# Kernel tuning notes

Hardware: AMD Instinct MI355X
Metric: run time of the kernel (lower is better)

## Reference

```python
import jax, jax.numpy as jnp
import numpy as np

B, C, M, NH, F_, W = 2, 8, 8, 8, 1024, 512  # batch, channels, attention_maps, heads, features, frames
HD = F_ // NH
EXP = 4


def _conv(x, w, b):
    y = jax.lax.conv_general_dilated(x, w, (1, 1), 'SAME',
                                     dimension_numbers=('NCHW', 'OIHW', 'NCHW'))
    return y + b[None, :, None, None]


def _rope(x):
    # x: (..., seq, d); lucidrains-style interleaved rotary embedding
    d, n = x.shape[-1], x.shape[-2]
    inv = 1.0 / (10000.0 ** (jnp.arange(0, d, 2, dtype=jnp.float32) / d))
    fr = jnp.repeat(jnp.arange(n, dtype=jnp.float32)[:, None] * inv[None, :], 2, axis=-1)
    cos, sin = jnp.cos(fr), jnp.sin(fr)
    xr = jnp.stack((-x[..., 1::2], x[..., 0::2]), axis=-1).reshape(x.shape)
    return x * cos + xr * sin


def _mcln(x, w, b, eps=1e-5):
    # MultichannelLayerNorm: normalize over features axis (axis=2 of B,C,F,W)
    mu = jnp.mean(x, axis=2, keepdims=True)
    var = jnp.var(x, axis=2, keepdims=True)
    return (x - mu) / jnp.sqrt(var + eps) * w[None, :, :, None] + b[None, :, :, None]


def _mclin(x, w_pw):
    # MultichannelLinear positionwise: per-channel matmul over features
    return jnp.einsum('bcfw,cgf->bcgw', x, w_pw)


def setup_inputs() -> dict:
    key = jax.random.key(0)
    ks = jax.random.split(key, 24)
    s = 0.02
    d = {
        'x': jax.random.normal(ks[0], (B, C, F_, W), jnp.float32),
        'prev_qk': jax.random.normal(ks[1], (B, M, NH, W, W), jnp.float32),
        'qconv_w': jax.random.normal(ks[2], (M, C, 3, 3), jnp.float32) * s,
        'qconv_b': jnp.zeros((M,), jnp.float32),
        'q_pw': jax.random.normal(ks[3], (M, F_, F_), jnp.float32) * s,
        'kconv_w': jax.random.normal(ks[4], (M, C, 3, 3), jnp.float32) * s,
        'kconv_b': jnp.zeros((M,), jnp.float32),
        'k_pw': jax.random.normal(ks[5], (M, F_, F_), jnp.float32) * s,
        'vconv_w': jax.random.normal(ks[6], (M, C, 3, 3), jnp.float32) * s,
        'vconv_b': jnp.zeros((M,), jnp.float32),
        'v_pw': jax.random.normal(ks[7], (M, F_, F_), jnp.float32) * s,
        'o_pw': jax.random.normal(ks[8], (M, F_, F_), jnp.float32) * s,
        'o_dw': jax.random.normal(ks[9], (M, M), jnp.float32) * s,
        'oproj_w': jax.random.normal(ks[10], (C, C + M, 3, 3), jnp.float32) * s,
        'oproj_b': jnp.zeros((C,), jnp.float32),
        'n1_w': jnp.ones((C, F_), jnp.float32),
        'n1_b': jnp.zeros((C, F_), jnp.float32),
        'c1_w': jax.random.normal(ks[11], (C * EXP, C, 3, 3), jnp.float32) * s,
        'c1_b': jnp.zeros((C * EXP,), jnp.float32),
        'c2_w': jax.random.normal(ks[12], (C, C * EXP, 3, 3), jnp.float32) * s,
        'c2_b': jnp.zeros((C,), jnp.float32),
        'n2_w': jnp.ones((C, F_), jnp.float32),
        'n2_b': jnp.zeros((C, F_), jnp.float32),
    }
    return d


def _encoder(x, prev_qk, qconv_w, qconv_b, q_pw, kconv_w, kconv_b, k_pw,
             vconv_w, vconv_b, v_pw, o_pw, o_dw, oproj_w, oproj_b,
             n1_w, n1_b, c1_w, c1_b, c2_w, c2_b, n2_w, n2_b):
    b, c, h, w = x.shape

    def heads(y):  # (B,M,F,W) -> (B,M,NH,W,HD)
        return y.transpose(0, 1, 3, 2).reshape(b, M, w, NH, HD).transpose(0, 1, 3, 2, 4)

    q = _rope(heads(_mclin(_conv(x, qconv_w, qconv_b), q_pw)))
    k = _rope(heads(_mclin(_conv(x, kconv_w, kconv_b), k_pw)))
    v = heads(_mclin(_conv(x, vconv_w, vconv_b), v_pw))

    qk = jnp.einsum('bmnqd,bmnkd->bmnqk', q, k) / jnp.sqrt(jnp.float32(h))
    qk = qk + prev_qk
    a = jnp.einsum('bmnqk,bmnkd->bmnqd', jax.nn.softmax(qk, axis=-1), v)
    a = a.transpose(0, 1, 3, 2, 4).reshape(b, M, w, NH * HD).transpose(0, 1, 3, 2)  # (B,M,F,W)
    a = jnp.einsum('bcfw,dc->bdfw', _mclin(a, o_pw), o_dw)  # depthwise o_linear
    z = _conv(jnp.concatenate((x, a), axis=1), oproj_w, oproj_b)

    hid = _mcln(x + z, n1_w, n1_b)  # dropout is identity in eval
    z2 = _conv(jax.nn.gelu(_conv(hid, c1_w, c1_b), approximate=False), c2_w, c2_b)
    out = _mcln(hid + z2, n2_w, n2_b)
    return out, qk


def reference(x, prev_qk, qconv_w, qconv_b, q_pw, kconv_w, kconv_b, k_pw,
              vconv_w, vconv_b, v_pw, o_pw, o_dw, oproj_w, oproj_b,
              n1_w, n1_b, c1_w, c1_b, c2_w, c2_b, n2_w, n2_b):
    out, qk = _encoder(x, prev_qk, qconv_w, qconv_b, q_pw, kconv_w, kconv_b, k_pw,
                       vconv_w, vconv_b, v_pw, o_pw, o_dw, oproj_w, oproj_b,
                       n1_w, n1_b, c1_w, c1_b, c2_w, c2_b, n2_w, n2_b)
    return (out, out, qk)
```

## Files before the change

### kernel.cpp

```cpp
#include <hip/hip_runtime.h>
#include <math.h>

#define B_ 2
#define C_ 8
#define M_ 8
#define NH_ 8
#define F_ 1024
#define W_ 512
#define HD_ 128
#define FW 524288L
#define PF_ 1026
#define PW_ 514

typedef __bf16 bf16_t;
typedef __bf16 bf16x8 __attribute__((ext_vector_type(8)));
typedef __bf16 bf16x4 __attribute__((ext_vector_type(4)));
typedef float f32x4 __attribute__((ext_vector_type(4)));

__device__ __forceinline__ void gload16(const void* g, void* l) {
    __builtin_amdgcn_global_load_lds(
        (const __attribute__((address_space(1))) unsigned int*)g,
        (__attribute__((address_space(3))) unsigned int*)l,
        16, 0, 0);
}

__device__ __forceinline__ float gelu_f(float v) {
    return 0.5f * v * (1.0f + erff(v * 0.70710678118f));
}

__device__ __forceinline__ void xcd_swz3(int& bx, int& by, int& bz) {
    const int nwg = gridDim.x * gridDim.y * gridDim.z;
    int orig = blockIdx.x + gridDim.x * (blockIdx.y + gridDim.y * blockIdx.z);
    orig = (orig & 7) * (nwg >> 3) + (orig >> 3);
    bx = orig % gridDim.x;
    int t = orig / gridDim.x;
    by = t % gridDim.y;
    bz = t / gridDim.y;
}

__global__ __launch_bounds__(256)
void prep_k(const float* __restrict__ q_pw, const float* __restrict__ k_pw,
            const float* __restrict__ v_pw, const float* __restrict__ o_pw,
            const float* __restrict__ x,
            const float* __restrict__ qw, const float* __restrict__ kw,
            const float* __restrict__ vw, const float* __restrict__ ow,
            const float* __restrict__ c1w, const float* __restrict__ c2w,
            const float* __restrict__ qb, const float* __restrict__ kb,
            const float* __restrict__ vb,
            bf16_t* __restrict__ W4, bf16_t* __restrict__ px,
            bf16_t* __restrict__ a_qkv, bf16_t* __restrict__ a_op,
            bf16_t* __restrict__ a_c1, bf16_t* __restrict__ a_c2,
            float* __restrict__ bias_qkv,
            bf16_t* __restrict__ p8a, bf16_t* __restrict__ p8b, bf16_t* __restrict__ p32)
{
    const int bid = blockIdx.x, tid = threadIdx.x;
    if (bid < 32768) {
        long i = (long)bid * 256 + tid;
        const int wsel = (int)(i >> 21);
        const long off = i & 2097151L;
        const float* src = (wsel == 0) ? q_pw : (wsel == 1) ? k_pw : (wsel == 2) ? v_pw : o_pw;
        float4 v = ((const float4*)src)[off];
        bf16x4 r = { (bf16_t)v.x, (bf16_t)v.y, (bf16_t)v.z, (bf16_t)v.w };
        *(bf16x4*)&W4[i * 4] = r;
    } else if (bid < 36889) {
        long i = (long)(bid - 32768) * 256 + tid;
        if (i >= (long)B_ * PF_ * PW_) return;
        int wc = (int)(i % PW_);
        long t = i / PW_;
        int fr = (int)(t % PF_);
        int b  = (int)(t / PF_);
        bf16x8 v = {};
        if (fr >= 1 && fr <= F_ && wc >= 1 && wc <= W_) {
            const float* s = x + (long)b * 8 * FW + (long)(fr - 1) * W_ + (wc - 1);
            #pragma unroll
            for (int c = 0; c < 8; ++c) v[c] = (bf16_t)s[c * FW];
        }
        *(bf16x8*)&px[i * 8] = v;
    } else if (bid < 36961) {
        int sub = bid - 36889;
        int mode = sub / 18;
        int i = (sub % 18) * 256 + tid;
        if (mode == 0) {
            if (i < 3072) {
                int k = i & 31, co = (i >> 5) & 31, df = i >> 10;
                int tap = k >> 3, ci = k & 7;
                float v = 0.f;
                if (tap < 3) {
                    if (co < 8)       v = qw[((co * 8 + ci) * 3 + df) * 3 + tap];
                    else if (co < 16) v = kw[(((co - 8) * 8 + ci) * 3 + df) * 3 + tap];
                    else if (co < 24) v = vw[(((co - 16) * 8 + ci) * 3 + df) * 3 + tap];
                }
                a_qkv[i] = (bf16_t)v;
            }
            if (i < 32) bias_qkv[i] = (i < 8) ? qb[i] : (i < 16) ? kb[i - 8] : (i < 24) ? vb[i - 16] : 0.f;
        } else if (mode == 1) {
            if (i < 3072) {
                int k = i & 63, co = (i >> 6) & 15, df = i >> 10;
                int src = k >> 5, r = k & 31, tap = r >> 3, ci = src * 8 + (r & 7);
                float v = 0.f;
                if (co < 8 && tap < 3) v = ow[((co * 16 + ci) * 3 + df) * 3 + tap];
                a_op[i] = (bf16_t)v;
            }
        } else if (mode == 2) {
            if (i < 3072) {
                int k = i & 31, co = (i >> 5) & 31, df = i >> 10;
                int tap = k >> 3, ci = k & 7;
                float v = (tap < 3) ? c1w[((co * 8 + ci) * 3 + df) * 3 + tap] : 0.f;
                a_c1[i] = (bf16_t)v;
            }
        } else {
            if (i < 4608) {
                int k = i % 96, co = (i / 96) & 15, df = i / (96 * 16);
                int tap = k >> 5, ci = k & 31;
                float v = (co < 8) ? c2w[((co * 32 + ci) * 3 + df) * 3 + tap] : 0.f;
                a_c2[i] = (bf16_t)v;
            }
        }
    } else {
        int i = (bid - 36961) * 256 + tid;
        if (i >= 2 * 3076) return;
        int b = i / 3076, p = i % 3076;
        int fr, wc;
        if (p < 514)       { fr = 0;    wc = p; }
        else if (p < 1028) { fr = 1025; wc = p - 514; }
        else if (p < 2052) { fr = 1 + (p - 1028); wc = 0; }
        else               { fr = 1 + (p - 2052); wc = 513; }
        long pix = ((long)b * PF_ + fr) * PW_ + wc;
        bf16x8 z = {};
        *(bf16x8*)&p8a[pix * 8] = z;
        *(bf16x8*)&p8b[pix * 8] = z;
        #pragma unroll
        for (int k = 0; k < 4; ++k) *(bf16x8*)&p32[pix * 32 + k * 8] = z;
    }
}

template<int CIN, int KSTEPS, int MFRAGS, int DUAL, int EPI, int RESBF>
__global__ __launch_bounds__(256)
void convg_k(const bf16_t* __restrict__ px0, const bf16_t* __restrict__ px1,
             const bf16_t* __restrict__ Ab, const float* __restrict__ bias,
             const void* __restrict__ resid, void* __restrict__ outp)
{
    const int f = blockIdx.y, b = blockIdx.z;
    const int tid = threadIdx.x, lane = tid & 63, wid = tid >> 6;
    const int l15 = lane & 15, l4 = lane >> 4;
    const int wbase = blockIdx.x * 256 + wid * 64;
    const int KW = KSTEPS * 32, M16 = MFRAGS * 16;

    bf16x8 af[3][MFRAGS][KSTEPS];
    #pragma unroll
    for (int df = 0; df < 3; ++df)
        #pragma unroll
        for (int mf = 0; mf < MFRAGS; ++mf)
            #pragma unroll
            for (int kk = 0; kk < KSTEPS; ++kk)
                af[df][mf][kk] = *(const bf16x8*)&Ab[(long)(df * M16 + mf * 16 + l15) * KW + kk * 32 + l4 * 8];

    f32x4 acc[MFRAGS][4];
    #pragma unroll
    for (int mf = 0; mf < MFRAGS; ++mf)
        #pragma unroll
        for (int nf = 0; nf < 4; ++nf)
            acc[mf][nf] = (f32x4){0.f, 0.f, 0.f, 0.f};

    #pragma unroll
    for (int df = 0; df < 3; ++df) {
        const long rowb = ((long)(b * PF_ + f + df)) * PW_ * CIN;
        #pragma unroll
        for (int nf = 0; nf < 4; ++nf) {
            const int wp = wbase + nf * 16 + l15;
            #pragma unroll
            for (int kk = 0; kk < KSTEPS; ++kk) {
                const bf16_t* src = (DUAL && kk == 1) ? px1 : px0;
                long addr = (CIN == 8) ? rowb + (long)(wp + l4) * 8
                                       : rowb + (long)(wp + kk) * 32 + l4 * 8;
                bf16x8 bv = *(const bf16x8*)&src[addr];
                #pragma unroll
                for (int mf = 0; mf < MFRAGS; ++mf)
                    acc[mf][nf] = __builtin_amdgcn_mfma_f32_16x16x32_bf16(
                        af[df][mf][kk], bv, acc[mf][nf], 0, 0, 0);
            }
        }
    }

    #pragma unroll
    for (int mf = 0; mf < MFRAGS; ++mf) {
        #pragma unroll
        for (int nf = 0; nf < 4; ++nf) {
            const int wp = wbase + nf * 16 + l15;
            if (EPI == 2) {
                const int cob = mf * 16 + l4 * 4;
                bf16x4 ov;
                #pragma unroll
                for (int r = 0; r < 4; ++r)
                    ov[r] = (bf16_t)gelu_f(acc[mf][nf][r] + bias[cob + r]);
                *(bf16x4*)&((bf16_t*)outp)[(((long)(b * PF_ + f + 1)) * PW_ + wp + 1) * 32 + cob] = ov;
            } else {
                #pragma unroll
                for (int r = 0; r < 4; ++r) {
                    const int co = mf * 16 + l4 * 4 + r;
                    float v = acc[mf][nf][r];
                    if (EPI == 0) {
                        if (co < 24)
                            ((bf16_t*)outp)[((long)(b * 24 + co)) * FW + (long)f * W_ + wp] = (bf16_t)(v + bias[co]);
                    } else {
                        if (co < 8) {
                            long oi = ((long)(b * 8 + co)) * FW + (long)f * W_ + wp;
                            float rv = RESBF ? (float)((const bf16_t*)resid)[oi]
                                             : ((const float*)resid)[oi];
                            ((bf16_t*)outp)[oi] = (bf16_t)(v + bias[co] + rv);
                        }
                    }
                }
            }
        }
    }
}

template<int OUTBF>
__global__ __launch_bounds__(256, 4)
void gemm_mfma_k(const bf16_t* __restrict__ Ab, const bf16_t* __restrict__ Bb,
                 void* __restrict__ Cb,
                 int Kdim, int lda, int ldb, int ldc,
                 long sA, long sB, long sC_hi, long sC_lo, int zdivC, int aMod)
{
    __shared__ bf16_t sAt[8192];
    __shared__ bf16_t sBt[8192];

    int bx, by, bz;
    xcd_swz3(bx, by, bz);
    const int z = bz;
    const int m0 = by * 128;
    const int n0 = bx * 128;
    const int tid = threadIdx.x;
    const int lane = tid & 63, wid = tid >> 6;
    const int wr = (wid >> 1) * 64, wc = (wid & 1) * 64;
    const int l15 = lane & 15, l4 = lane >> 4;

    const bf16_t* A = Ab + (long)(z % aMod) * sA;
    const bf16_t* B = Bb + (long)z * sB;

    f32x4 acc[4][4];
    #pragma unroll
    for (int m = 0; m < 4; ++m)
        #pragma unroll
        for (int n = 0; n < 4; ++n)
            acc[m][n] = (f32x4){0.f, 0.f, 0.f, 0.f};

    const int grow = wid * 8 + (lane >> 3);
    const int gslot = lane & 7;

    for (int k0 = 0; k0 < Kdim; k0 += 64) {
        __syncthreads();
        #pragma unroll
        for (int r = 0; r < 4; ++r) {
            const int row = r * 32 + grow;
            gload16(A + (long)(m0 + row) * lda + k0 + ((gslot ^ (row & 7)) << 3),
                    sAt + r * 2048 + wid * 512);
        }
        #pragma unroll
        for (int r = 0; r < 4; ++r) {
            const int row = r * 32 + grow;
            gload16(B + (long)(n0 + row) * ldb + k0 + ((gslot ^ (row & 7)) << 3),
                    sBt + r * 2048 + wid * 512);
        }
        __syncthreads();

        bf16x8 afr[4][2], bfr[4][2];
        #pragma unroll
        for (int m = 0; m < 4; ++m) {
            const int row = wr + m * 16 + l15, swz = row & 7;
            afr[m][0] = *(const bf16x8*)&sAt[row * 64 + ((l4 ^ swz) << 3)];
            afr[m][1] = *(const bf16x8*)&sAt[row * 64 + (((4 + l4) ^ swz) << 3)];
        }
        #pragma unroll
        for (int n = 0; n < 4; ++n) {
            const int row = wc + n * 16 + l15, swz = row & 7;
            bfr[n][0] = *(const bf16x8*)&sBt[row * 64 + ((l4 ^ swz) << 3)];
            bfr[n][1] = *(const bf16x8*)&sBt[row * 64 + (((4 + l4) ^ swz) << 3)];
        }
        #pragma unroll
        for (int kk = 0; kk < 2; ++kk)
            #pragma unroll
            for (int m = 0; m < 4; ++m)
                #pragma unroll
                for (int n = 0; n < 4; ++n)
                    acc[m][n] = __builtin_amdgcn_mfma_f32_16x16x32_bf16(
                        afr[m][kk], bfr[n][kk], acc[m][n], 0, 0, 0);
    }

    const long zc = (long)(z / zdivC) * sC_hi + (long)(z % zdivC) * sC_lo;
    #pragma unroll
    for (int m = 0; m < 4; ++m) {
        #pragma unroll
        for (int n = 0; n < 4; ++n) {
            #pragma unroll
            for (int r = 0; r < 4; ++r) {
                int row = m0 + wr + m * 16 + l4 * 4 + r;
                int col = n0 + wc + n * 16 + l15;
                float v = acc[m][n][r];
                long cidx = zc + (long)row * ldc + col;
                if (OUTBF) ((bf16_t*)Cb)[cidx] = (bf16_t)v;
                else       ((float*)Cb)[cidx]  = v;
            }
        }
    }
}

__global__ __launch_bounds__(256)
void qkgemm_k(const bf16_t* __restrict__ QR, const bf16_t* __restrict__ KR,
              float* __restrict__ Cb, const float* __restrict__ prevb,
              float* __restrict__ stats)
{
    __shared__ bf16_t sAt[8192];
    __shared__ bf16_t sBt[8192];
    __shared__ float red[2][128][2];

    int bx, by, bz;
    xcd_swz3(bx, by, bz);
    const int z = bz;
    const int m0 = by * 128;
    const int n0 = bx * 128;
    const int tid = threadIdx.x;
    const int lane = tid & 63, wid = tid >> 6;
    const int wr = (wid >> 1) * 64, wc = (wid & 1) * 64;
    const int l15 = lane & 15, l4 = lane >> 4;

    const bf16_t* A = QR + (long)z * 65536L;
    const bf16_t* B = KR + (long)z * 65536L;

    f32x4 acc[4][4];
    #pragma unroll
    for (int m = 0; m < 4; ++m)
        #pragma unroll
        for (int n = 0; n < 4; ++n)
            acc[m][n] = (f32x4){0.f, 0.f, 0.f, 0.f};

    const int grow = wid * 8 + (lane >> 3);
    const int gslot = lane & 7;

    for (int k0 = 0; k0 < 128; k0 += 64) {
        __syncthreads();
        #pragma unroll
        for (int r = 0; r < 4; ++r) {
            const int row = r * 32 + grow;
            gload16(A + (long)(m0 + row) * 128 + k0 + ((gslot ^ (row & 7)) << 3),
                    sAt + r * 2048 + wid * 512);
        }
        #pragma unroll
        for (int r = 0; r < 4; ++r) {
            const int row = r * 32 + grow;
            gload16(B + (long)(n0 + row) * 128 + k0 + ((gslot ^ (row & 7)) << 3),
                    sBt + r * 2048 + wid * 512);
        }
        __syncthreads();

        bf16x8 afr[4][2], bfr[4][2];
        #pragma unroll
        for (int m = 0; m < 4; ++m) {
            const int row = wr + m * 16 + l15, swz = row & 7;
            afr[m][0] = *(const bf16x8*)&sAt[row * 64 + ((l4 ^ swz) << 3)];
            afr[m][1] = *(const bf16x8*)&sAt[row * 64 + (((4 + l4) ^ swz) << 3)];
        }
        #pragma unroll
        for (int n = 0; n < 4; ++n) {
            const int row = wc + n * 16 + l15, swz = row & 7;
            bfr[n][0] = *(const bf16x8*)&sBt[row * 64 + ((l4 ^ swz) << 3)];
            bfr[n][1] = *(const bf16x8*)&sBt[row * 64 + (((4 + l4) ^ swz) << 3)];
        }
        #pragma unroll
        for (int kk = 0; kk < 2; ++kk)
            #pragma unroll
            for (int m = 0; m < 4; ++m)
                #pragma unroll
                for (int n = 0; n < 4; ++n)
                    acc[m][n] = __builtin_amdgcn_mfma_f32_16x16x32_bf16(
                        afr[m][kk], bfr[n][kk], acc[m][n], 0, 0, 0);
    }

    const long zc = (long)z * 262144L;
    #pragma unroll
    for (int m = 0; m < 4; ++m) {
        #pragma unroll
        for (int n = 0; n < 4; ++n) {
            #pragma unroll
            for (int r = 0; r < 4; ++r) {
                int row = m0 + wr + m * 16 + l4 * 4 + r;
                int col = n0 + wc + n * 16 + l15;
                float v = acc[m][n][r] * 0.03125f + prevb[zc + (long)row * 512 + col];
                acc[m][n][r] = v;
                Cb[zc + (long)row * 512 + col] = v;
            }
        }
    }
    #pragma unroll
    for (int m = 0; m < 4; ++m) {
        #pragma unroll
        for (int r = 0; r < 4; ++r) {
            float mx = -1e30f;
            #pragma unroll
            for (int n = 0; n < 4; ++n) mx = fmaxf(mx, acc[m][n][r]);
            #pragma unroll
            for (int o = 1; o <= 8; o <<= 1) mx = fmaxf(mx, __shfl_xor(mx, o, 64));
            float se = 0.f;
            #pragma unroll
            for (int n = 0; n < 4; ++n) se += __expf(acc[m][n][r] - mx);
            #pragma unroll
            for (int o = 1; o <= 8; o <<= 1) se += __shfl_xor(se, o, 64);
            if (l15 == 0) {
                int row = wr + m * 16 + l4 * 4 + r;
                red[wid & 1][row][0] = mx;
                red[wid & 1][row][1] = se;
            }
        }
    }
    __syncthreads();
    if (tid < 128) {
        float ma = red[0][tid][0], sa = red[0][tid][1];
        float mb = red[1][tid][0], sb = red[1][tid][1];
        float M = fmaxf(ma, mb);
        float S = sa * __expf(ma - M) + sb * __expf(mb - M);
        *(float2*)&stats[(((long)z * 4 + bx) * 512 + m0 + tid) * 2] = make_float2(M, S);
    }
}

__global__ __launch_bounds__(256, 4)
void qkvgemm_k(const bf16_t* __restrict__ W4, const bf16_t* __restrict__ XT,
               bf16_t* __restrict__ outp )
{
    __shared__ bf16_t sAt[8192];
    __shared__ bf16_t sBt[8192];

    int bx, by, bz;
    xcd_swz3(bx, by, bz);
    const int zz = bz;
    const int path = zz >> 4, bm = zz & 15;
    const bf16_t* A = W4 + (long)(path * 8 + (bm & 7)) * 1048576L;
    const bf16_t* B = XT + (long)zz * FW;
    const int m0 = by * 128;
    const int n0 = bx * 128;
    const int tid = threadIdx.x;
    const int lane = tid & 63, wid = tid >> 6;
    const int wr = (wid >> 1) * 64, wc = (wid & 1) * 64;
    const int l15 = lane & 15, l4 = lane >> 4;

    f32x4 acc[4][4];
    #pragma unroll
    for (int m = 0; m < 4; ++m)
        #pragma unroll
        for (int n = 0; n < 4; ++n)
            acc[m][n] = (f32x4){0.f, 0.f, 0.f, 0.f};

    const int grow = wid * 8 + (lane >> 3);
    const int gslot = lane & 7;

    for (int k0 = 0; k0 < 1024; k0 += 64) {
        __syncthreads();
        #pragma unroll
        for (int r = 0; r < 4; ++r) {
            const int row = r * 32 + grow;
            gload16(A + (long)(m0 + row) * 1024 + k0 + ((gslot ^ (row & 7)) << 3),
                    sAt + r * 2048 + wid * 512);
        }
        #pragma unroll
        for (int r = 0; r < 4; ++r) {
            const int row = r * 32 + grow;
            gload16(B + (long)(n0 + row) * 1024 + k0 + ((gslot ^ (row & 7)) << 3),
                    sBt + r * 2048 + wid * 512);
        }
        __syncthreads();

        bf16x8 afr[4][2], bfr[4][2];
        #pragma unroll
        for (int m = 0; m < 4; ++m) {
            const int row = wr + m * 16 + l15, swz = row & 7;
            afr[m][0] = *(const bf16x8*)&sAt[row * 64 + ((l4 ^ swz) << 3)];
            afr[m][1] = *(const bf16x8*)&sAt[row * 64 + (((4 + l4) ^ swz) << 3)];
        }
        #pragma unroll
        for (int n = 0; n < 4; ++n) {
            const int row = wc + n * 16 + l15, swz = row & 7;
            bfr[n][0] = *(const bf16x8*)&sBt[row * 64 + ((l4 ^ swz) << 3)];
            bfr[n][1] = *(const bf16x8*)&sBt[row * 64 + (((4 + l4) ^ swz) << 3)];
        }
        #pragma unroll
        for (int kk = 0; kk < 2; ++kk)
            #pragma unroll
            for (int m = 0; m < 4; ++m)
                #pragma unroll
                for (int n = 0; n < 4; ++n)
                    acc[m][n] = __builtin_amdgcn_mfma_f32_16x16x32_bf16(
                        afr[m][kk], bfr[n][kk], acc[m][n], 0, 0, 0);
    }

    if (path < 2) {
        const long base = (long)path * 8388608L + (((long)bm * 8 + by) * 512L) * 128L;
        #pragma unroll
        for (int m = 0; m < 4; ++m) {
            const int d0 = wr + m * 16 + l4 * 4;
            const float inv0 = __expf(-(float)(d0 >> 1) * 0.14391156507f);
            const float inv1 = __expf(-(float)((d0 >> 1) + 1) * 0.14391156507f);
            #pragma unroll
            for (int n = 0; n < 4; ++n) {
                const int col = n0 + wc + n * 16 + l15;
                float s0, c0, s1, c1;
                __sincosf((float)col * inv0, &s0, &c0);
                __sincosf((float)col * inv1, &s1, &c1);
                float v0 = acc[m][n][0], v1 = acc[m][n][1];
                float v2 = acc[m][n][2], v3 = acc[m][n][3];
                bf16x4 ov = { (bf16_t)(v0 * c0 - v1 * s0), (bf16_t)(v1 * c0 + v0 * s0),
                              (bf16_t)(v2 * c1 - v3 * s1), (bf16_t)(v3 * c1 + v2 * s1) };
                *(bf16x4*)&outp[base + (long)col * 128 + d0] = ov;
            }
        }
    } else {
        const long base = 16777216L + (long)bm * FW;
        #pragma unroll
        for (int m = 0; m < 4; ++m)
            #pragma unroll
            for (int n = 0; n < 4; ++n)
                #pragma unroll
                for (int r = 0; r < 4; ++r) {
                    int row = m0 + wr + m * 16 + l4 * 4 + r;
                    int col = n0 + wc + n * 16 + l15;
                    outp[base + (long)row * 512 + col] = (bf16_t)acc[m][n][r];
                }
    }
}

__global__ __launch_bounds__(256, 4)
void smpv_k(const float* __restrict__ S, const bf16_t* __restrict__ VL,
            const float* __restrict__ stats, bf16_t* __restrict__ AT)
{
    __shared__ bf16_t sP[8192];
    __shared__ bf16_t sB[8192];
    __shared__ float smax[128], sinv[128];

    int bx, by, bz;
    xcd_swz3(bx, by, bz);
    const int z = bz;
    const int m0 = bx * 128;
    const float* Sb = S + (long)z * 262144L;
    const bf16_t* Bb = VL + (long)z * 65536L;
    const int tid = threadIdx.x, lane = tid & 63, wid = tid >> 6;
    const int l15 = lane & 15, l4 = lane >> 4;
    const int wr = (wid >> 1) * 64, wc = (wid & 1) * 64;

    if (tid < 128) {
        float M = -1e30f, Ssum = 0.f;
        #pragma unroll
        for (int kb = 0; kb < 4; ++kb) {
            float2 p = *(const float2*)&stats[(((long)z * 4 + kb) * 512 + m0 + tid) * 2];
            float nm = fmaxf(M, p.x);
            Ssum = Ssum * __expf(M - nm) + p.y * __expf(p.x - nm);
            M = nm;
        }
        smax[tid] = M;
        sinv[tid] = 1.0f / Ssum;
    }
    __syncthreads();

    f32x4 acc[4][4];
    #pragma unroll
    for (int m = 0; m < 4; ++m)
        #pragma unroll
        for (int n = 0; n < 4; ++n)
            acc[m][n] = (f32x4){0.f, 0.f, 0.f, 0.f};

    const int grow = wid * 8 + (lane >> 3);
    const int gslot = lane & 7;
    const int prow0 = tid >> 4, pl = tid & 15;

    for (int kt = 0; kt < 512; kt += 64) {
        __syncthreads();
        #pragma unroll
        for (int p = 0; p < 8; ++p) {
            const int row = p * 16 + prow0;
            float4 v = *(const float4*)(Sb + (long)(m0 + row) * 512 + kt + pl * 4);
            float mr = smax[row];
            bf16x4 e = { (bf16_t)__expf(v.x - mr), (bf16_t)__expf(v.y - mr),
                         (bf16_t)__expf(v.z - mr), (bf16_t)__expf(v.w - mr) };
            *(bf16x4*)((char*)sP + row * 128 + ((((pl >> 1) ^ (row & 7))) << 4) + (pl & 1) * 8) = e;
        }
        #pragma unroll
        for (int r = 0; r < 4; ++r) {
            const int row = r * 32 + grow;
            gload16(Bb + (long)row * 512 + kt + ((gslot ^ (row & 7)) << 3),
                    sB + r * 2048 + wid * 512);
        }
        __syncthreads();

        bf16x8 afr[4][2], bfr[4][2];
        #pragma unroll
        for (int m = 0; m < 4; ++m) {
            const int row = wr + m * 16 + l15, swz = row & 7;
            afr[m][0] = *(const bf16x8*)&sP[row * 64 + ((l4 ^ swz) << 3)];
            afr[m][1] = *(const bf16x8*)&sP[row * 64 + (((4 + l4) ^ swz) << 3)];
        }
        #pragma unroll
        for (int n = 0; n < 4; ++n) {
            const int row = wc + n * 16 + l15, swz = row & 7;
            bfr[n][0] = *(const bf16x8*)&sB[row * 64 + ((l4 ^ swz) << 3)];
            bfr[n][1] = *(const bf16x8*)&sB[row * 64 + (((4 + l4) ^ swz) << 3)];
        }
        #pragma unroll
        for (int kk = 0; kk < 2; ++kk)
            #pragma unroll
            for (int m = 0; m < 4; ++m)
                #pragma unroll
                for (int n = 0; n < 4; ++n)
                    acc[m][n] = __builtin_amdgcn_mfma_f32_16x16x32_bf16(
                        afr[m][kk], bfr[n][kk], acc[m][n], 0, 0, 0);
    }

    const long base = (long)(z >> 3) * FW + (long)(z & 7) * 128L;
    #pragma unroll
    for (int m = 0; m < 4; ++m) {
        #pragma unroll
        for (int n = 0; n < 4; ++n) {
            #pragma unroll
            for (int r = 0; r < 4; ++r) {
                const int row = wr + m * 16 + l4 * 4 + r;
                const int col = wc + n * 16 + l15;
                float v = acc[m][n][r] * sinv[row];
                AT[base + (long)(m0 + row) * 1024 + col] = (bf16_t)v;
            }
        }
    }
}

__global__ __launch_bounds__(256)
void tcvt_k(const bf16_t* __restrict__ in, bf16_t* __restrict__ outp)
{
    __shared__ float tile[32][33];
    const int w0 = blockIdx.x * 32, f0 = blockIdx.y * 32;
    const int z = blockIdx.z;
    const int path = z >> 4, bm = z & 15;
    const int inSlice = (bm >> 3) * 24 + path * 8 + (bm & 7);
    const long ibase = (long)inSlice * FW;
    const long obase = (long)z * FW;
    const int tx = threadIdx.x & 31, ty = threadIdx.x >> 5;
    #pragma unroll
    for (int i = 0; i < 4; ++i)
        tile[ty + i * 8][tx] = (float)in[ibase + (long)(f0 + ty + i * 8) * W_ + w0 + tx];
    __syncthreads();
    #pragma unroll
    for (int i = 0; i < 4; ++i)
        outp[obase + (long)(w0 + ty + i * 8) * F_ + f0 + tx] = (bf16_t)tile[tx][ty + i * 8];
}

__global__ __launch_bounds__(256)
void odw_k(const bf16_t* __restrict__ t, const float* __restrict__ dw, bf16_t* __restrict__ px)
{
    long i = (long)blockIdx.x * 256 + threadIdx.x;
    int w = (int)(i & (W_ - 1));
    long q = i >> 9;
    int f = (int)(q & (F_ - 1));
    int b = (int)(q >> 10);
    const bf16_t* s = t + (long)b * 8 * FW + (long)f * W_ + w;
    float tv[8];
    #pragma unroll
    for (int c = 0; c < 8; ++c) tv[c] = (float)s[c * FW];
    bf16x8 o;
    #pragma unroll
    for (int d = 0; d < 8; ++d) {
        float a = 0.f;
        #pragma unroll
        for (int c = 0; c < 8; ++c) a += tv[c] * dw[d * 8 + c];
        o[d] = (bf16_t)a;
    }
    *(bf16x8*)&px[(((long)b * PF_ + f + 1) * PW_ + w + 1) * 8] = o;
}

template<typename TIN, int O1BF>
__global__ __launch_bounds__(256)
void mcln_k(const TIN* __restrict__ in, const float* __restrict__ gam,
            const float* __restrict__ bet, void* __restrict__ o1, float* __restrict__ o2,
            bf16_t* __restrict__ px)
{
    int wi = threadIdx.x & 31, fg = threadIdx.x >> 5;
    int w0 = blockIdx.x * 32;
    int c = blockIdx.y, b = blockIdx.z;
    long base = ((long)b * C_ + c) * FW + w0 + wi;
    float s = 0.f, q = 0.f;
    for (int f = fg; f < F_; f += 8) {
        float v = (float)in[base + (long)f * W_];
        s += v; q += v * v;
    }
    __shared__ float rs[8][33], rq[8][33];
    __shared__ float mu_s[32], inv_s[32];
    rs[fg][wi] = s; rq[fg][wi] = q;
    __syncthreads();
    if (fg == 0) {
        float ts = 0.f, tq = 0.f;
        for (int g = 0; g < 8; ++g) { ts += rs[g][wi]; tq += rq[g][wi]; }
        float mu = ts * (1.0f / F_);
        float var = tq * (1.0f / F_) - mu * mu;
        mu_s[wi] = mu;
        inv_s[wi] = rsqrtf(var + 1e-5f);
    }
    __syncthreads();
    float mu = mu_s[wi], inv = inv_s[wi];
    for (int f = fg; f < F_; f += 8) {
        float v = (float)in[base + (long)f * W_];
        float r = (v - mu) * inv * gam[c * F_ + f] + bet[c * F_ + f];
        long oi = base + (long)f * W_;
        if (O1BF) ((bf16_t*)o1)[oi] = (bf16_t)r;
        else      ((float*)o1)[oi]  = r;
        if (o2) o2[oi] = r;
        if (px) px[(((long)b * PF_ + f + 1) * PW_ + (w0 + wi) + 1) * 8 + c] = (bf16_t)r;
    }
}

extern "C" void kernel_launch(void* const* d_in, const int* in_sizes, int n_in,
                              void* d_out, int out_size, void* d_ws, size_t ws_size,
                              hipStream_t stream) {
    (void)in_sizes; (void)n_in; (void)out_size; (void)ws_size;
    const float* x        = (const float*)d_in[0];
    const float* prev_qk  = (const float*)d_in[1];
    const float* qconv_w  = (const float*)d_in[2];
    const float* qconv_b  = (const float*)d_in[3];
    const float* q_pw     = (const float*)d_in[4];
    const float* kconv_w  = (const float*)d_in[5];
    const float* kconv_b  = (const float*)d_in[6];
    const float* k_pw     = (const float*)d_in[7];
    const float* vconv_w  = (const float*)d_in[8];
    const float* vconv_b  = (const float*)d_in[9];
    const float* v_pw     = (const float*)d_in[10];
    const float* o_pw     = (const float*)d_in[11];
    const float* o_dw     = (const float*)d_in[12];
    const float* oproj_w  = (const float*)d_in[13];
    const float* oproj_b  = (const float*)d_in[14];
    const float* n1_w     = (const float*)d_in[15];
    const float* n1_b     = (const float*)d_in[16];
    const float* c1_w     = (const float*)d_in[17];
    const float* c1_b     = (const float*)d_in[18];
    const float* c2_w     = (const float*)d_in[19];
    const float* c2_b     = (const float*)d_in[20];
    const float* n2_w     = (const float*)d_in[21];
    const float* n2_b     = (const float*)d_in[22];

    float* out    = (float*)d_out;
    float* qk_out = out + 16777216L;

    char* wsb = (char*)d_ws;
    bf16_t* PX8  = (bf16_t*)(wsb + 0L);
    bf16_t* W4   = (bf16_t*)(wsb + 16876032L);
    bf16_t* QR   = (bf16_t*)(wsb + 83984896L);
    bf16_t* KR   = (bf16_t*)(wsb + 100762112L);
    bf16_t* VL   = (bf16_t*)(wsb + 117539328L);
    bf16_t* XT48 = (bf16_t*)(wsb + 134316544L);
    bf16_t* HIDb = (bf16_t*)(wsb + 134316544L);
    bf16_t* QKV  = (bf16_t*)(wsb + 184648192L);
    bf16_t* AT   = (bf16_t*)(wsb + 184648192L);
    bf16_t* F1b  = (bf16_t*)(wsb + 201425408L);
    bf16_t* PRE  = (bf16_t*)(wsb + 218202624L);
    bf16_t* PXA2 = (bf16_t*)(wsb + 234979840L);
    bf16_t* PXH  = (bf16_t*)(wsb + 251855616L);
    bf16_t* PXC1 = (bf16_t*)(wsb + 268731392L);
    bf16_t* ABQ  = (bf16_t*)(wsb + 336233984L);
    bf16_t* ABO  = (bf16_t*)(wsb + 336233984L + 16384L);
    bf16_t* ABC1 = (bf16_t*)(wsb + 336233984L + 32768L);
    bf16_t* ABC2 = (bf16_t*)(wsb + 336233984L + 49152L);
    float*  BQKV = (float*) (wsb + 336233984L + 65536L);
    float*  STAT = (float*) (wsb + 336365056L);

    const dim3 cvgrid(2, F_, B_);
    const dim3 tgrid(16, 32, 48);

    prep_k<<<36986, 256, 0, stream>>>(q_pw, k_pw, v_pw, o_pw, x,
                                      qconv_w, kconv_w, vconv_w, oproj_w, c1_w, c2_w,
                                      qconv_b, kconv_b, vconv_b,
                                      W4, PX8, ABQ, ABO, ABC1, ABC2, BQKV,
                                      PXA2, PXH, PXC1);

    convg_k<8, 1, 2, 0, 0, 0><<<cvgrid, 256, 0, stream>>>(PX8, nullptr, ABQ, BQKV, nullptr, QKV);

    tcvt_k<<<tgrid, 256, 0, stream>>>(QKV, XT48);
    qkvgemm_k<<<dim3(4, 8, 48), 256, 0, stream>>>(W4, XT48, QR);

    qkgemm_k<<<dim3(4, 4, 128), 256, 0, stream>>>(QR, KR, qk_out, prev_qk, STAT);
    smpv_k<<<dim3(4, 1, 128), 256, 0, stream>>>(qk_out, VL, STAT, AT);

    gemm_mfma_k<1><<<dim3(4, 8, 16), 256, 0, stream>>>(W4 + 25165824L, AT, F1b,
        F_, F_, F_, W_, 1048576L, 524288L, 524288L, 0L, 1, 8);
    odw_k<<<4096, 256, 0, stream>>>(F1b, o_dw, PXA2);

    convg_k<8, 2, 1, 1, 1, 0><<<cvgrid, 256, 0, stream>>>(PX8, PXA2, ABO, oproj_b, x, PRE);

    mcln_k<bf16_t, 1><<<dim3(16, 8, 2), 256, 0, stream>>>(PRE, n1_w, n1_b, HIDb, nullptr, PXH);

    convg_k<8, 1, 2, 0, 2, 0><<<cvgrid, 256, 0, stream>>>(PXH, nullptr, ABC1, c1_b, nullptr, PXC1);
    convg_k<32, 3, 1, 0, 1, 1><<<cvgrid, 256, 0, stream>>>(PXC1, nullptr, ABC2, c2_b, HIDb, PRE);
    mcln_k<bf16_t, 0><<<dim3(16, 8, 2), 256, 0, stream>>>(PRE, n2_w, n2_b, out, out + 8388608L, nullptr);
}
```

Measured before the change: 653.7 us.

## Fuse QK gemm, softmax stats and PV gemm into one attention kernel

Merges the QK^T+prev_qk kernel and the softmax-times-V kernel into a single attn_k. Each block now loops over all four key chunks for its 128 query rows, keeps a running max/sum in shared memory, then reads the scores back from global memory to build P and multiply by V. This drops one launch and the stats buffer round trip. In exchange the grid shrinks from 2048 blocks to 512 for the QK phase, which cuts parallelism, and the scores are still written out and re-read.

```diff
diff --git a/kernel.cpp b/kernel.cpp
--- a/kernel.cpp
+++ b/kernel.cpp
@@ -306,123 +306,6 @@
     }
 }
 
-__global__ __launch_bounds__(256)
-void qkgemm_k(const bf16_t* __restrict__ QR, const bf16_t* __restrict__ KR,
-              float* __restrict__ Cb, const float* __restrict__ prevb,
-              float* __restrict__ stats)
-{
-    __shared__ bf16_t sAt[8192];
-    __shared__ bf16_t sBt[8192];
-    __shared__ float red[2][128][2];
-
-    int bx, by, bz;
-    xcd_swz3(bx, by, bz);
-    const int z = bz;
-    const int m0 = by * 128;
-    const int n0 = bx * 128;
-    const int tid = threadIdx.x;
-    const int lane = tid & 63, wid = tid >> 6;
-    const int wr = (wid >> 1) * 64, wc = (wid & 1) * 64;
-    const int l15 = lane & 15, l4 = lane >> 4;
-
-    const bf16_t* A = QR + (long)z * 65536L;
-    const bf16_t* B = KR + (long)z * 65536L;
-
-    f32x4 acc[4][4];
-    #pragma unroll
-    for (int m = 0; m < 4; ++m)
-        #pragma unroll
-        for (int n = 0; n < 4; ++n)
-            acc[m][n] = (f32x4){0.f, 0.f, 0.f, 0.f};
-
-    const int grow = wid * 8 + (lane >> 3);
-    const int gslot = lane & 7;
-
-    for (int k0 = 0; k0 < 128; k0 += 64) {
-        __syncthreads();
-        #pragma unroll
-        for (int r = 0; r < 4; ++r) {
-            const int row = r * 32 + grow;
-            gload16(A + (long)(m0 + row) * 128 + k0 + ((gslot ^ (row & 7)) << 3),
-                    sAt + r * 2048 + wid * 512);
-        }
-        #pragma unroll
-        for (int r = 0; r < 4; ++r) {
-            const int row = r * 32 + grow;
-            gload16(B + (long)(n0 + row) * 128 + k0 + ((gslot ^ (row & 7)) << 3),
-                    sBt + r * 2048 + wid * 512);
-        }
-        __syncthreads();
-
-        bf16x8 afr[4][2], bfr[4][2];
-        #pragma unroll
-        for (int m = 0; m < 4; ++m) {
-            const int row = wr + m * 16 + l15, swz = row & 7;
-            afr[m][0] = *(const bf16x8*)&sAt[row * 64 + ((l4 ^ swz) << 3)];
-            afr[m][1] = *(const bf16x8*)&sAt[row * 64 + (((4 + l4) ^ swz) << 3)];
-        }
-        #pragma unroll
-        for (int n = 0; n < 4; ++n) {
-            const int row = wc + n * 16 + l15, swz = row & 7;
-            bfr[n][0] = *(const bf16x8*)&sBt[row * 64 + ((l4 ^ swz) << 3)];
-            bfr[n][1] = *(const bf16x8*)&sBt[row * 64 + (((4 + l4) ^ swz) << 3)];
-        }
-        #pragma unroll
-        for (int kk = 0; kk < 2; ++kk)
-            #pragma unroll
-            for (int m = 0; m < 4; ++m)
-                #pragma unroll
-                for (int n = 0; n < 4; ++n)
-                    acc[m][n] = __builtin_amdgcn_mfma_f32_16x16x32_bf16(
-                        afr[m][kk], bfr[n][kk], acc[m][n], 0, 0, 0);
-    }
-
-    const long zc = (long)z * 262144L;
-    #pragma unroll
-    for (int m = 0; m < 4; ++m) {
-        #pragma unroll
-        for (int n = 0; n < 4; ++n) {
-            #pragma unroll
-            for (int r = 0; r < 4; ++r) {
-                int row = m0 + wr + m * 16 + l4 * 4 + r;
-                int col = n0 + wc + n * 16 + l15;
-                float v = acc[m][n][r] * 0.03125f + prevb[zc + (long)row * 512 + col];
-                acc[m][n][r] = v;
-                Cb[zc + (long)row * 512 + col] = v;
-            }
-        }
-    }
-    #pragma unroll
-    for (int m = 0; m < 4; ++m) {
-        #pragma unroll
-        for (int r = 0; r < 4; ++r) {
-            float mx = -1e30f;
-            #pragma unroll
-            for (int n = 0; n < 4; ++n) mx = fmaxf(mx, acc[m][n][r]);
-            #pragma unroll
-            for (int o = 1; o <= 8; o <<= 1) mx = fmaxf(mx, __shfl_xor(mx, o, 64));
-            float se = 0.f;
-            #pragma unroll
-            for (int n = 0; n < 4; ++n) se += __expf(acc[m][n][r] - mx);
-            #pragma unroll
-            for (int o = 1; o <= 8; o <<= 1) se += __shfl_xor(se, o, 64);
-            if (l15 == 0) {
-                int row = wr + m * 16 + l4 * 4 + r;
-                red[wid & 1][row][0] = mx;
-                red[wid & 1][row][1] = se;
-            }
-        }
-    }
-    __syncthreads();
-    if (tid < 128) {
-        float ma = red[0][tid][0], sa = red[0][tid][1];
-        float mb = red[1][tid][0], sb = red[1][tid][1];
-        float M = fmaxf(ma, mb);
-        float S = sa * __expf(ma - M) + sb * __expf(mb - M);
-        *(float2*)&stats[(((long)z * 4 + bx) * 512 + m0 + tid) * 2] = make_float2(M, S);
-    }
-}
-
 __global__ __launch_bounds__(256, 4)
 void qkvgemm_k(const bf16_t* __restrict__ W4, const bf16_t* __restrict__ XT,
                bf16_t* __restrict__ outp )
@@ -527,47 +410,139 @@
     }
 }
 
-__global__ __launch_bounds__(256, 4)
-void smpv_k(const float* __restrict__ S, const bf16_t* __restrict__ VL,
-            const float* __restrict__ stats, bf16_t* __restrict__ AT)
+__global__ __launch_bounds__(256, 2)
+void attn_k(const bf16_t* __restrict__ QR, const bf16_t* __restrict__ KR,
+            const bf16_t* __restrict__ VL, const float* __restrict__ prevb,
+            float* __restrict__ Sout, bf16_t* __restrict__ AT)
 {
-    __shared__ bf16_t sP[8192];
+    __shared__ bf16_t sA[8192];
     __shared__ bf16_t sB[8192];
-    __shared__ float smax[128], sinv[128];
+    __shared__ float red[2][128][2];
+    __shared__ float Mrun[128], Srun[128];
 
     int bx, by, bz;
     xcd_swz3(bx, by, bz);
+    (void)by;
     const int z = bz;
     const int m0 = bx * 128;
-    const float* Sb = S + (long)z * 262144L;
-    const bf16_t* Bb = VL + (long)z * 65536L;
+    const bf16_t* Qb = QR + (long)z * 65536L;
+    const bf16_t* Kb = KR + (long)z * 65536L;
+    const bf16_t* Vb = VL + (long)z * 65536L;
+    const float* prev = prevb + (long)z * 262144L;
+    float* Sb = Sout + (long)z * 262144L;
+
     const int tid = threadIdx.x, lane = tid & 63, wid = tid >> 6;
     const int l15 = lane & 15, l4 = lane >> 4;
     const int wr = (wid >> 1) * 64, wc = (wid & 1) * 64;
-
-    if (tid < 128) {
-        float M = -1e30f, Ssum = 0.f;
-        #pragma unroll
-        for (int kb = 0; kb < 4; ++kb) {
-            float2 p = *(const float2*)&stats[(((long)z * 4 + kb) * 512 + m0 + tid) * 2];
-            float nm = fmaxf(M, p.x);
-            Ssum = Ssum * __expf(M - nm) + p.y * __expf(p.x - nm);
-            M = nm;
-        }
-        smax[tid] = M;
-        sinv[tid] = 1.0f / Ssum;
-    }
-    __syncthreads();
-
-    f32x4 acc[4][4];
-    #pragma unroll
-    for (int m = 0; m < 4; ++m)
-        #pragma unroll
-        for (int n = 0; n < 4; ++n)
-            acc[m][n] = (f32x4){0.f, 0.f, 0.f, 0.f};
-
     const int grow = wid * 8 + (lane >> 3);
     const int gslot = lane & 7;
+
+    if (tid < 128) { Mrun[tid] = -1e30f; Srun[tid] = 0.f; }
+
+    for (int kc = 0; kc < 4; ++kc) {
+        f32x4 acc[4][4];
+        #pragma unroll
+        for (int m = 0; m < 4; ++m)
+            #pragma unroll
+            for (int n = 0; n < 4; ++n)
+                acc[m][n] = (f32x4){0.f, 0.f, 0.f, 0.f};
+
+        #pragma unroll
+        for (int k0 = 0; k0 < 128; k0 += 64) {
+            __syncthreads();
+            #pragma unroll
+            for (int r = 0; r < 4; ++r) {
+                const int row = r * 32 + grow;
+                gload16(Qb + (long)(m0 + row) * 128 + k0 + ((gslot ^ (row & 7)) << 3),
+                        sA + r * 2048 + wid * 512);
+            }
+            #pragma unroll
+            for (int r = 0; r < 4; ++r) {
+                const int row = r * 32 + grow;
+                gload16(Kb + (long)(kc * 128 + row) * 128 + k0 + ((gslot ^ (row & 7)) << 3),
+                        sB + r * 2048 + wid * 512);
+            }
+            __syncthreads();
+
+            bf16x8 afr[4][2], bfr[4][2];
+            #pragma unroll
+            for (int m = 0; m < 4; ++m) {
+                const int row = wr + m * 16 + l15, swz = row & 7;
+                afr[m][0] = *(const bf16x8*)&sA[row * 64 + ((l4 ^ swz) << 3)];
+                afr[m][1] = *(const bf16x8*)&sA[row * 64 + (((4 + l4) ^ swz) << 3)];
+            }
+            #pragma unroll
+            for (int n = 0; n < 4; ++n) {
+                const int row = wc + n * 16 + l15, swz = row & 7;
+                bfr[n][0] = *(const bf16x8*)&sB[row * 64 + ((l4 ^ swz) << 3)];
+                bfr[n][1] = *(const bf16x8*)&sB[row * 64 + (((4 + l4) ^ swz) << 3)];
+            }
+            #pragma unroll
+            for (int kk = 0; kk < 2; ++kk)
+                #pragma unroll
+                for (int m = 0; m < 4; ++m)
+                    #pragma unroll
+                    for (int n = 0; n < 4; ++n)
+                        acc[m][n] = __builtin_amdgcn_mfma_f32_16x16x32_bf16(
+                            afr[m][kk], bfr[n][kk], acc[m][n], 0, 0, 0);
+        }
+
+        #pragma unroll
+        for (int m = 0; m < 4; ++m) {
+            #pragma unroll
+            for (int n = 0; n < 4; ++n) {
+                #pragma unroll
+                for (int r = 0; r < 4; ++r) {
+                    int row = m0 + wr + m * 16 + l4 * 4 + r;
+                    int col = kc * 128 + wc + n * 16 + l15;
+                    float v = acc[m][n][r] * 0.03125f + prev[(long)row * 512 + col];
+                    acc[m][n][r] = v;
+                    Sb[(long)row * 512 + col] = v;
+                }
+            }
+        }
+        #pragma unroll
+        for (int m = 0; m < 4; ++m) {
+            #pragma unroll
+            for (int r = 0; r < 4; ++r) {
+                float mx = -1e30f;
+                #pragma unroll
+                for (int n = 0; n < 4; ++n) mx = fmaxf(mx, acc[m][n][r]);
+                #pragma unroll
+                for (int o = 1; o <= 8; o <<= 1) mx = fmaxf(mx, __shfl_xor(mx, o, 64));
+                float se = 0.f;
+                #pragma unroll
+                for (int n = 0; n < 4; ++n) se += __expf(acc[m][n][r] - mx);
+                #pragma unroll
+                for (int o = 1; o <= 8; o <<= 1) se += __shfl_xor(se, o, 64);
+                if (l15 == 0) {
+                    int row = wr + m * 16 + l4 * 4 + r;
+                    red[wid & 1][row][0] = mx;
+                    red[wid & 1][row][1] = se;
+                }
+            }
+        }
+        __syncthreads();
+        if (tid < 128) {
+            float ma = red[0][tid][0], sa = red[0][tid][1];
+            float mb = red[1][tid][0], sb = red[1][tid][1];
+            float mt = fmaxf(ma, mb);
+            float st = sa * __expf(ma - mt) + sb * __expf(mb - mt);
+            float M0 = Mrun[tid], S0 = Srun[tid];
+            float M1 = fmaxf(M0, mt);
+            Srun[tid] = S0 * __expf(M0 - M1) + st * __expf(mt - M1);
+            Mrun[tid] = M1;
+        }
+    }
+    __syncthreads();
+
+    f32x4 oacc[4][4];
+    #pragma unroll
+    for (int m = 0; m < 4; ++m)
+        #pragma unroll
+        for (int n = 0; n < 4; ++n)
+            oacc[m][n] = (f32x4){0.f, 0.f, 0.f, 0.f};
+
     const int prow0 = tid >> 4, pl = tid & 15;
 
     for (int kt = 0; kt < 512; kt += 64) {
@@ -576,15 +551,15 @@
         for (int p = 0; p < 8; ++p) {
             const int row = p * 16 + prow0;
             float4 v = *(const float4*)(Sb + (long)(m0 + row) * 512 + kt + pl * 4);
-            float mr = smax[row];
+            float mr = Mrun[row];
             bf16x4 e = { (bf16_t)__expf(v.x - mr), (bf16_t)__expf(v.y - mr),
                          (bf16_t)__expf(v.z - mr), (bf16_t)__expf(v.w - mr) };
-            *(bf16x4*)((char*)sP + row * 128 + ((((pl >> 1) ^ (row & 7))) << 4) + (pl & 1) * 8) = e;
+            *(bf16x4*)((char*)sA + row * 128 + ((((pl >> 1) ^ (row & 7))) << 4) + (pl & 1) * 8) = e;
         }
         #pragma unroll
         for (int r = 0; r < 4; ++r) {
             const int row = r * 32 + grow;
-            gload16(Bb + (long)row * 512 + kt + ((gslot ^ (row & 7)) << 3),
+            gload16(Vb + (long)row * 512 + kt + ((gslot ^ (row & 7)) << 3),
                     sB + r * 2048 + wid * 512);
         }
         __syncthreads();
@@ -593,8 +568,8 @@
         #pragma unroll
         for (int m = 0; m < 4; ++m) {
             const int row = wr + m * 16 + l15, swz = row & 7;
-            afr[m][0] = *(const bf16x8*)&sP[row * 64 + ((l4 ^ swz) << 3)];
-            afr[m][1] = *(const bf16x8*)&sP[row * 64 + (((4 + l4) ^ swz) << 3)];
+            afr[m][0] = *(const bf16x8*)&sA[row * 64 + ((l4 ^ swz) << 3)];
+            afr[m][1] = *(const bf16x8*)&sA[row * 64 + (((4 + l4) ^ swz) << 3)];
         }
         #pragma unroll
         for (int n = 0; n < 4; ++n) {
@@ -608,8 +583,8 @@
             for (int m = 0; m < 4; ++m)
                 #pragma unroll
                 for (int n = 0; n < 4; ++n)
-                    acc[m][n] = __builtin_amdgcn_mfma_f32_16x16x32_bf16(
-                        afr[m][kk], bfr[n][kk], acc[m][n], 0, 0, 0);
+                    oacc[m][n] = __builtin_amdgcn_mfma_f32_16x16x32_bf16(
+                        afr[m][kk], bfr[n][kk], oacc[m][n], 0, 0, 0);
     }
 
     const long base = (long)(z >> 3) * FW + (long)(z & 7) * 128L;
@@ -621,7 +596,7 @@
             for (int r = 0; r < 4; ++r) {
                 const int row = wr + m * 16 + l4 * 4 + r;
                 const int col = wc + n * 16 + l15;
-                float v = acc[m][n][r] * sinv[row];
+                float v = oacc[m][n][r] / Srun[row];
                 AT[base + (long)(m0 + row) * 1024 + col] = (bf16_t)v;
             }
         }
@@ -762,7 +737,6 @@
     bf16_t* ABC1 = (bf16_t*)(wsb + 336233984L + 32768L);
     bf16_t* ABC2 = (bf16_t*)(wsb + 336233984L + 49152L);
     float*  BQKV = (float*) (wsb + 336233984L + 65536L);
-    float*  STAT = (float*) (wsb + 336365056L);
 
     const dim3 cvgrid(2, F_, B_);
     const dim3 tgrid(16, 32, 48);
@@ -778,8 +752,7 @@
     tcvt_k<<<tgrid, 256, 0, stream>>>(QKV, XT48);
     qkvgemm_k<<<dim3(4, 8, 48), 256, 0, stream>>>(W4, XT48, QR);
 
-    qkgemm_k<<<dim3(4, 4, 128), 256, 0, stream>>>(QR, KR, qk_out, prev_qk, STAT);
-    smpv_k<<<dim3(4, 1, 128), 256, 0, stream>>>(qk_out, VL, STAT, AT);
+    attn_k<<<dim3(4, 1, 128), 256, 0, stream>>>(QR, KR, VL, prev_qk, qk_out, AT);
 
     gemm_mfma_k<1><<<dim3(4, 8, 16), 256, 0, stream>>>(W4 + 25165824L, AT, F1b,
         F_, F_, F_, W_, 1048576L, 524288L, 524288L, 0L, 1, 8);
```

After: 613.1 us. -6.2%, faster.
